# Performance work log

Measured on AMD Instinct MI355X. Metric: run time of the kernel, lower is better.

The kernel has to match this reference:

```python
import math
import jax, jax.numpy as jnp
import numpy as np

B, L, D, H, NL, V = 4, 1024, 1024, 16, 8, 32000
HD = D // H
EPS = 1e-5


def _sinusoidal_pe(length, dim):
    pos = jnp.arange(length, dtype=jnp.float32)[:, None]
    div = jnp.exp(jnp.arange(0, dim, 2, dtype=jnp.float32) * (-math.log(10000.0) / dim))
    pe = jnp.zeros((length, dim), dtype=jnp.float32)
    pe = pe.at[:, 0::2].set(jnp.sin(pos * div))
    pe = pe.at[:, 1::2].set(jnp.cos(pos * div))
    return pe


def _layer_norm(x, scale, bias):
    mu = jnp.mean(x, axis=-1, keepdims=True)
    var = jnp.mean(jnp.square(x - mu), axis=-1, keepdims=True)
    return (x - mu) * jax.lax.rsqrt(var + EPS) * scale + bias


def setup_inputs() -> dict:
    key = jax.random.key(0)
    ks = jax.random.split(key, 10)
    std = 0.02
    p = {
        "idx": jax.random.randint(ks[0], (B, L), 0, V),
        "emb": jax.random.normal(ks[1], (V, D), jnp.float32) * std,
        # per-layer stacked params (leading dim NL)
        "ln1_s": jnp.ones((NL, D), jnp.float32),
        "ln1_b": jnp.zeros((NL, D), jnp.float32),
        "wq": jax.random.normal(ks[2], (NL, D, D), jnp.float32) * std,
        "wk": jax.random.normal(ks[3], (NL, D, D), jnp.float32) * std,
        "wv": jax.random.normal(ks[4], (NL, D, D), jnp.float32) * std,
        "wo": jax.random.normal(ks[5], (NL, D, D), jnp.float32) * std,
        "ln2_s": jnp.ones((NL, D), jnp.float32),
        "ln2_b": jnp.zeros((NL, D), jnp.float32),
        "w1": jax.random.normal(ks[6], (NL, D, 4 * D), jnp.float32) * std,
        "b1": jnp.zeros((NL, 4 * D), jnp.float32),
        "w2": jax.random.normal(ks[7], (NL, 4 * D, D), jnp.float32) * std,
        "b2": jnp.zeros((NL, D), jnp.float32),
        "lnf_s": jnp.ones((D,), jnp.float32),
        "lnf_b": jnp.zeros((D,), jnp.float32),
        "head": jax.random.normal(ks[8], (D, V), jnp.float32) * std,
    }
    return p


def _forward(idx, emb, ln1_s, ln1_b, wq, wk, wv, wo, ln2_s, ln2_b, w1, b1, w2, b2, lnf_s, lnf_b, head):
    x = emb[idx] + _sinusoidal_pe(L, D)[None]  # [B,L,D]
    causal = jnp.tril(jnp.ones((L, L), dtype=bool))  # [L,L]
    neg_inf = jnp.float32(-jnp.inf)

    def block(x, p):
        (l1s, l1b, Wq, Wk, Wv, Wo, l2s, l2b, W1, B1, W2, B2) = p
        h = _layer_norm(x, l1s, l1b)
        q = (h @ Wq).reshape(B, L, H, HD)
        k = (h @ Wk).reshape(B, L, H, HD)
        v = (h @ Wv).reshape(B, L, H, HD)
        att = jnp.einsum("bihd,bjhd->bhij", q, k) / math.sqrt(HD)
        att = jnp.where(causal, att, neg_inf)
        att = jax.nn.softmax(att, axis=-1)
        y = jnp.einsum("bhij,bjhd->bihd", att, v).reshape(B, L, D)
        x = x + y @ Wo
        h = _layer_norm(x, l2s, l2b)
        x = x + jax.nn.gelu(h @ W1 + B1, approximate=False) @ W2 + B2
        return x, None

    params = (ln1_s, ln1_b, wq, wk, wv, wo, ln2_s, ln2_b, w1, b1, w2, b2)
    x, _ = jax.lax.scan(block, x, params)
    x = _layer_norm(x, lnf_s, lnf_b)
    return x @ head  # [B,L,V]


def reference(idx, emb, ln1_s, ln1_b, wq, wk, wv, wo, ln2_s, ln2_b, w1, b1, w2, b2, lnf_s, lnf_b, head):
    return _forward(idx, emb, ln1_s, ln1_b, wq, wk, wv, wo, ln2_s, ln2_b, w1, b1, w2, b2, lnf_s, lnf_b, head)
```

## Files before the change

kernel.cpp:

```cpp
#include <hip/hip_runtime.h>
#include <hip/hip_bf16.h>
#include <math.h>

typedef __bf16 bf16_t;
typedef __attribute__((ext_vector_type(8))) __bf16 bf16x8;
typedef __attribute__((ext_vector_type(4))) float f32x4;

#define B_  4
#define L_  1024
#define D_  1024
#define H_  16
#define HD_ 64
#define NL_ 8
#define V_  32000
#define FF_ 4096

__global__ __launch_bounds__(256) void embed_kernel(const int* __restrict__ idx,
                                                    const float* __restrict__ emb,
                                                    float* __restrict__ x) {
  int token = blockIdx.x;
  int l = token & (L_ - 1);
  int id = idx[token];
  const float* erow = emb + (size_t)id * D_;
  float* xrow = x + (size_t)token * D_;
  int d0 = threadIdx.x * 4;
#pragma unroll
  for (int j = 0; j < 4; ++j) {
    int d = d0 + j;
    int i = d >> 1;
    float freq = expf((float)(2 * i) * (-9.210340371976184f / (float)D_));
    float ang = (float)l * freq;
    float pe = (d & 1) ? cosf(ang) : sinf(ang);
    xrow[d] = erow[d] + pe;
  }
}

__global__ __launch_bounds__(256) void ln_kernel(const float* __restrict__ x,
                                                 const float* __restrict__ gamma,
                                                 const float* __restrict__ beta,
                                                 bf16_t* __restrict__ out) {
  int row = blockIdx.x;
  int t = threadIdx.x;
  float4 v = ((const float4*)(x + (size_t)row * D_))[t];
  float va[4] = {v.x, v.y, v.z, v.w};
  float s = va[0] + va[1] + va[2] + va[3];
  float ss = va[0]*va[0] + va[1]*va[1] + va[2]*va[2] + va[3]*va[3];
#pragma unroll
  for (int m = 1; m < 64; m <<= 1) {
    s  += __shfl_xor(s, m);
    ss += __shfl_xor(ss, m);
  }
  __shared__ float red[8];
  int wid = t >> 6, lane = t & 63;
  if (lane == 0) { red[wid] = s; red[4 + wid] = ss; }
  __syncthreads();
  s  = red[0] + red[1] + red[2] + red[3];
  ss = red[4] + red[5] + red[6] + red[7];
  float mu  = s * (1.0f / D_);
  float var = fmaxf(ss * (1.0f / D_) - mu * mu, 0.0f);
  float rstd = rsqrtf(var + 1e-5f);
  int d0 = t * 4;
  bf16_t* orow = out + (size_t)row * D_ + d0;
#pragma unroll
  for (int j = 0; j < 4; ++j) {
    int d = d0 + j;
    orow[j] = (bf16_t)((va[j] - mu) * rstd * gamma[d] + beta[d]);
  }
}

__global__ void transpose_k(const float* __restrict__ in, size_t base,
                            bf16_t* __restrict__ out, int K, int N, int ldin) {
  __shared__ bf16_t tile[32][33];
  int n0 = blockIdx.x * 32, k0 = blockIdx.y * 32;
#pragma unroll
  for (int r = 0; r < 4; ++r) {
    int kk = threadIdx.y + r * 8;
    tile[kk][threadIdx.x] = (bf16_t)in[base + (size_t)(k0 + kk) * ldin + n0 + threadIdx.x];
  }
  __syncthreads();
#pragma unroll
  for (int r = 0; r < 4; ++r) {
    int nn = threadIdx.y + r * 8;
    out[(size_t)(n0 + nn) * K + k0 + threadIdx.x] = tile[threadIdx.x][nn];
  }
}

__global__ void transpose_qkv(const float* __restrict__ wq,
                              const float* __restrict__ wk,
                              const float* __restrict__ wv, size_t base,
                              bf16_t* __restrict__ out) {
  const float* in = (blockIdx.z == 0) ? wq : (blockIdx.z == 1) ? wk : wv;
  __shared__ bf16_t tile[32][33];
  int n0 = blockIdx.x * 32, k0 = blockIdx.y * 32;
#pragma unroll
  for (int r = 0; r < 4; ++r) {
    int kk = threadIdx.y + r * 8;
    tile[kk][threadIdx.x] = (bf16_t)in[base + (size_t)(k0 + kk) * D_ + n0 + threadIdx.x];
  }
  __syncthreads();
  bf16_t* o = out + (size_t)blockIdx.z * D_ * D_;
#pragma unroll
  for (int r = 0; r < 4; ++r) {
    int nn = threadIdx.y + r * 8;
    o[(size_t)(n0 + nn) * D_ + k0 + threadIdx.x] = tile[threadIdx.x][nn];
  }
}

__device__ __forceinline__ void gload_lds16(const bf16_t* g, bf16_t* lds) {
  __builtin_amdgcn_global_load_lds(
      (const __attribute__((address_space(1))) void*)g,
      (__attribute__((address_space(3))) void*)(void*)lds,
      16, 0, 0);
}

__device__ __forceinline__ void remap_block(int& bn, int& bm) {
  const int gx = gridDim.x, gy = gridDim.y;
  int lin = blockIdx.y * gx + blockIdx.x;
  int nwg = gx * gy;
  int q8 = nwg >> 3, r8 = nwg & 7;
  int xcd = lin & 7, pos = lin >> 3;
  int wg = (xcd < r8 ? xcd * (q8 + 1) : r8 * (q8 + 1) + (xcd - r8) * q8) + pos;
  if ((gy & 7) == 0) {
    int per = gx << 3;
    int grp = wg / per, win = wg % per;
    bm = (grp << 3) + (win & 7);
    bn = win >> 3;
  } else { bn = wg % gx; bm = wg / gx; }
}

template <int EPI>
__global__ __launch_bounds__(256) void gemm_bt_kernel(
    const bf16_t* __restrict__ A, const bf16_t* __restrict__ Bt,
    bf16_t* __restrict__ outb, float* __restrict__ outf,
    const float* __restrict__ bias, int M, int Nst, int K, int col0) {
  int bn, bm; remap_block(bn, bm);
  const int tid = threadIdx.x, wid = tid >> 6, lane = tid & 63;
  const int wm = wid >> 1, wn = wid & 1;
  const int l15 = lane & 15, l4 = lane >> 4;

  __shared__ __align__(16) bf16_t As[128 * 32];
  __shared__ __align__(16) bf16_t Bs[128 * 32];

  f32x4 acc[4][4] = {};

  const bf16_t* Ablk = A  + (size_t)(bm * 128) * K;
  const bf16_t* Bblk = Bt + (size_t)(bn * 128) * K;
  const int srow = lane >> 2;
  const int skof = (lane & 3) * 8;

  for (int k0 = 0; k0 < K; k0 += 32) {
#pragma unroll
    for (int c = 0; c < 2; ++c) {
      int chunk = wid * 2 + c;
      int row = chunk * 16 + srow;
      gload_lds16(Ablk + (size_t)row * K + k0 + skof, As + chunk * 512);
      gload_lds16(Bblk + (size_t)row * K + k0 + skof, Bs + chunk * 512);
    }
    __syncthreads();

    bf16x8 af[4], bfv[4];
#pragma unroll
    for (int i = 0; i < 4; ++i)
      af[i] = *(const bf16x8*)(As + (wm * 64 + i * 16 + l15) * 32 + l4 * 8);
#pragma unroll
    for (int j = 0; j < 4; ++j)
      bfv[j] = *(const bf16x8*)(Bs + (wn * 64 + j * 16 + l15) * 32 + l4 * 8);
#pragma unroll
    for (int i = 0; i < 4; ++i)
#pragma unroll
      for (int j = 0; j < 4; ++j)
        acc[i][j] = __builtin_amdgcn_mfma_f32_16x16x32_bf16(af[i], bfv[j], acc[i][j], 0, 0, 0);
    __syncthreads();
  }

  const int row_base = bm * 128 + wm * 64;
  const int col_base = col0 + bn * 128 + wn * 64 + l15;
#pragma unroll
  for (int i = 0; i < 4; ++i) {
#pragma unroll
    for (int j = 0; j < 4; ++j) {
      int col = col_base + j * 16;
#pragma unroll
      for (int r = 0; r < 4; ++r) {
        int row = row_base + i * 16 + l4 * 4 + r;
        float val = acc[i][j][r];
        if (EPI == 1) {
          outf[(size_t)row * Nst + col] += val;
        } else {
          outf[(size_t)row * Nst + col] += val + bias[col];
        }
      }
    }
  }
}

template <int EPI>
__global__ __launch_bounds__(512, 2) void gemm256_kernel(
    const bf16_t* __restrict__ A, const bf16_t* __restrict__ Bt,
    bf16_t* __restrict__ outb, float* __restrict__ outf,
    const float* __restrict__ bias, int M, int Nst, int K, int col0) {
  int bn, bm; remap_block(bn, bm);
  const int tid = threadIdx.x, wid = tid >> 6, lane = tid & 63;
  const int wm = wid >> 2, wn = wid & 3;
  const int l15 = lane & 15, l4 = lane >> 4;

  __shared__ __align__(16) bf16_t smem[65536];

  f32x4 acc[8][4] = {};

  const bf16_t* Ab = A  + (size_t)(bm * 256) * K;
  const bf16_t* Bb = Bt + (size_t)(bn * 256) * K;
  const int NT = K >> 6;

  const int srow = tid >> 3;
  const int sx8  = tid & 7;
  const int xrd  = l15 & 7;

  auto stage_rows = [&](int t, int mat, int R) {
    const bf16_t* g = mat ? Bb : Ab;
    bf16_t* l = smem + (t & 1) * 32768 + mat * 16384 + R * 64;
    int row = R + srow;
    int gs  = sx8 ^ (row & 7);
    gload_lds16(g + (size_t)row * K + t * 64 + gs * 8, l + wid * 512);
  };
  auto stA_SP0 = [&](int t) { stage_rows(t, 0, 0);   stage_rows(t, 0, 128); };
  auto stA_SP1 = [&](int t) { stage_rows(t, 0, 64);  stage_rows(t, 0, 192); };
  auto stB_H0  = [&](int t) { stage_rows(t, 1, 0);   stage_rows(t, 1, 64);  };
  auto stB_H1  = [&](int t) { stage_rows(t, 1, 128); stage_rows(t, 1, 192); };

  stA_SP0(0); stB_H0(0); stA_SP1(0); stB_H1(0);
  stA_SP0(1); stB_H0(1); stA_SP1(1);
  asm volatile("s_waitcnt vmcnt(6)" ::: "memory");
  __builtin_amdgcn_s_barrier();

  bf16x8 af[4][2], bfr[4][2];

  auto rdB = [&](const bf16_t* sB, int nh) {
#pragma unroll
    for (int n = 0; n < 2; ++n)
#pragma unroll
      for (int ks = 0; ks < 2; ++ks)
        bfr[nh * 2 + n][ks] = *(const bf16x8*)(sB + (wn * 64 + (nh * 2 + n) * 16 + l15) * 64
                                                  + ((ks * 4 + l4) ^ xrd) * 8);
  };
  auto rdA = [&](const bf16_t* sA, int mh) {
#pragma unroll
    for (int m = 0; m < 4; ++m)
#pragma unroll
      for (int ks = 0; ks < 2; ++ks)
        af[m][ks] = *(const bf16x8*)(sA + (wm * 128 + mh * 64 + m * 16 + l15) * 64
                                        + ((ks * 4 + l4) ^ xrd) * 8);
  };
  auto mma = [&](int mh, int nh) {
    asm volatile("s_waitcnt lgkmcnt(0)" ::: "memory");
    __builtin_amdgcn_sched_barrier(0);
    __builtin_amdgcn_s_setprio(1);
#pragma unroll
    for (int m = 0; m < 4; ++m)
#pragma unroll
      for (int n = 0; n < 2; ++n)
#pragma unroll
        for (int ks = 0; ks < 2; ++ks)
          acc[mh * 4 + m][nh * 2 + n] = __builtin_amdgcn_mfma_f32_16x16x32_bf16(
              af[m][ks], bfr[nh * 2 + n][ks], acc[mh * 4 + m][nh * 2 + n], 0, 0, 0);
    __builtin_amdgcn_s_setprio(0);
  };

  const int NI = NT >> 1;
  for (int it = 0; it < NI; ++it) {
    const int T0 = 2 * it, T1 = 2 * it + 1;
    const bool pre = (it + 1 < NI);
    const bf16_t* sA0 = smem;
    const bf16_t* sB0 = smem + 16384;
    const bf16_t* sA1 = smem + 32768;
    const bf16_t* sB1 = smem + 49152;

    rdB(sB0, 0); rdA(sA0, 0);
    stB_H1(T1);
    __builtin_amdgcn_s_barrier();
    mma(0, 0);
    __builtin_amdgcn_s_barrier();
    rdB(sB0, 1);
    if (pre) stA_SP0(T0 + 2);
    __builtin_amdgcn_s_barrier();
    mma(0, 1);
    __builtin_amdgcn_s_barrier();
    rdA(sA0, 1);
    if (pre) stB_H0(T0 + 2);
    __builtin_amdgcn_s_barrier();
    mma(1, 0);
    __builtin_amdgcn_s_barrier();
    if (pre) stA_SP1(T0 + 2);
    __builtin_amdgcn_s_barrier();
    mma(1, 1);
    if (pre) { asm volatile("s_waitcnt vmcnt(6)" ::: "memory"); }
    else     { asm volatile("s_waitcnt vmcnt(0)" ::: "memory"); }
    __builtin_amdgcn_s_barrier();

    rdB(sB1, 0); rdA(sA1, 0);
    if (pre) stB_H1(T0 + 2);
    __builtin_amdgcn_s_barrier();
    mma(0, 0);
    __builtin_amdgcn_s_barrier();
    rdB(sB1, 1);
    if (pre) stA_SP0(T1 + 2);
    __builtin_amdgcn_s_barrier();
    mma(0, 1);
    __builtin_amdgcn_s_barrier();
    rdA(sA1, 1);
    if (pre) stB_H0(T1 + 2);
    __builtin_amdgcn_s_barrier();
    mma(1, 0);
    __builtin_amdgcn_s_barrier();
    if (pre) stA_SP1(T1 + 2);
    __builtin_amdgcn_s_barrier();
    mma(1, 1);
    if (pre) { asm volatile("s_waitcnt vmcnt(6)" ::: "memory"); }
    __builtin_amdgcn_s_barrier();
  }

  const int row_base = bm * 256 + wm * 128;
#pragma unroll
  for (int m = 0; m < 8; ++m) {
#pragma unroll
    for (int n = 0; n < 4; ++n) {
      int colg = bn * 256 + wn * 64 + n * 16 + l15;
#pragma unroll
      for (int r = 0; r < 4; ++r) {
        int row = row_base + m * 16 + l4 * 4 + r;
        float val = acc[m][n][r];
        if (EPI == 4) {
          outf[(size_t)row * Nst + col0 + colg] = val;
        } else if (EPI == 2) {
          int col = col0 + colg;
          float v2 = val + bias[col];
          v2 = 0.5f * v2 * (1.0f + erff(v2 * 0.7071067811865475f));
          outb[(size_t)row * Nst + col] = (bf16_t)v2;
        } else {
          int buf = colg >> 10;
          int lc  = colg & 1023;
          (outb + (size_t)buf * 4194304)[(size_t)row * 1024 + lc] = (bf16_t)val;
        }
      }
    }
  }
}

__global__ __launch_bounds__(256) void attn_kernel(
    const bf16_t* __restrict__ q, const bf16_t* __restrict__ k,
    const bf16_t* __restrict__ v, bf16_t* __restrict__ y) {
  int bid = blockIdx.x;
  int qt = bid & 15;
  int h  = (bid >> 4) & (H_ - 1);
  int b  = bid >> 8;
  int tid = threadIdx.x, wid = tid >> 6, lane = tid & 63;
  int l15 = lane & 15, l4 = lane >> 4;

  __shared__ __align__(16) bf16_t Ks[64 * 72];
  __shared__ __align__(16) bf16_t Vs[64 * 72];
  __shared__ __align__(16) bf16_t Ps[4][16 * 72];

  const int qrow0 = qt * 64 + wid * 16;
  const size_t bh = ((size_t)b * L_ * H_ + h) * HD_;

  bf16x8 qf[2];
#pragma unroll
  for (int c = 0; c < 2; ++c)
    qf[c] = *(const bf16x8*)(q + bh + (size_t)(qrow0 + l15) * (H_ * HD_) + c * 32 + l4 * 8);

  float m_r[4] = {-INFINITY, -INFINITY, -INFINITY, -INFINITY};
  float l_r[4] = {0.f, 0.f, 0.f, 0.f};
  f32x4 oacc[4] = {};

  for (int kt = 0; kt <= qt; ++kt) {
    __syncthreads();
    int kbase = kt * 64;
#pragma unroll
    for (int s = 0; s < 2; ++s) {
      int seg = s * 256 + tid;
      int j = seg >> 3;
      int dof = (seg & 7) * 8;
      const size_t src = bh + (size_t)(kbase + j) * (H_ * HD_) + dof;
      *(bf16x8*)(Ks + j * 72 + dof) = *(const bf16x8*)(k + src);
      bf16x8 vv = *(const bf16x8*)(v + src);
      int colb = (j + dof) & 63;
#pragma unroll
      for (int jj = 0; jj < 8; ++jj) Vs[(dof + jj) * 72 + colb] = vv[jj];
    }
    __syncthreads();

    f32x4 sacc[4] = {};
#pragma unroll
    for (int c = 0; c < 2; ++c) {
#pragma unroll
      for (int t = 0; t < 4; ++t) {
        bf16x8 kf = *(const bf16x8*)(Ks + (t * 16 + l15) * 72 + c * 32 + l4 * 8);
        sacc[t] = __builtin_amdgcn_mfma_f32_16x16x32_bf16(qf[c], kf, sacc[t], 0, 0, 0);
      }
    }

    float tmax[4] = {-INFINITY, -INFINITY, -INFINITY, -INFINITY};
#pragma unroll
    for (int t = 0; t < 4; ++t) {
#pragma unroll
      for (int r = 0; r < 4; ++r) {
        float sv = sacc[t][r] * 0.125f;
        int kj = kbase + t * 16 + l15;
        int qi = qrow0 + l4 * 4 + r;
        if (kj > qi) sv = -INFINITY;
        sacc[t][r] = sv;
        tmax[r] = fmaxf(tmax[r], sv);
      }
    }
#pragma unroll
    for (int r = 0; r < 4; ++r) {
#pragma unroll
      for (int md = 1; md < 16; md <<= 1)
        tmax[r] = fmaxf(tmax[r], __shfl_xor(tmax[r], md));
    }
    float alpha[4], tsum[4];
#pragma unroll
    for (int r = 0; r < 4; ++r) {
      float mn = fmaxf(m_r[r], tmax[r]);
      alpha[r] = expf(m_r[r] - mn);
      m_r[r] = mn;
      tsum[r] = 0.f;
    }
#pragma unroll
    for (int t = 0; t < 4; ++t) {
#pragma unroll
      for (int r = 0; r < 4; ++r) {
        float p = expf(sacc[t][r] - m_r[r]);
        tsum[r] += p;
        Ps[wid][(l4 * 4 + r) * 72 + t * 16 + l15] = (bf16_t)p;
      }
    }
#pragma unroll
    for (int r = 0; r < 4; ++r) {
#pragma unroll
      for (int md = 1; md < 16; md <<= 1)
        tsum[r] += __shfl_xor(tsum[r], md);
      l_r[r] = l_r[r] * alpha[r] + tsum[r];
    }
#pragma unroll
    for (int t = 0; t < 4; ++t)
#pragma unroll
      for (int r = 0; r < 4; ++r)
        oacc[t][r] *= alpha[r];

#pragma unroll
    for (int c = 0; c < 2; ++c) {
      bf16x8 pf = *(const bf16x8*)(&Ps[wid][l15 * 72 + c * 32 + l4 * 8]);
#pragma unroll
      for (int t = 0; t < 4; ++t) {
        int d = t * 16 + l15;
        int jb = c * 32 + l4 * 8;
        bf16x8 vf = *(const bf16x8*)(Vs + d * 72 + ((jb + (d & 56)) & 63));
        oacc[t] = __builtin_amdgcn_mfma_f32_16x16x32_bf16(pf, vf, oacc[t], 0, 0, 0);
      }
    }
  }

#pragma unroll
  for (int t = 0; t < 4; ++t) {
#pragma unroll
    for (int r = 0; r < 4; ++r) {
      int row = qrow0 + l4 * 4 + r;
      int d = t * 16 + l15;
      y[bh + (size_t)row * (H_ * HD_) + d] = (bf16_t)(oacc[t][r] / l_r[r]);
    }
  }
}

extern "C" void kernel_launch(void* const* d_in, const int* in_sizes, int n_in,
                              void* d_out, int out_size, void* d_ws, size_t ws_size,
                              hipStream_t stream) {
  (void)in_sizes; (void)n_in; (void)out_size;
  const int*   idx   = (const int*)d_in[0];
  const float* emb   = (const float*)d_in[1];
  const float* ln1_s = (const float*)d_in[2];
  const float* ln1_b = (const float*)d_in[3];
  const float* wq    = (const float*)d_in[4];
  const float* wk    = (const float*)d_in[5];
  const float* wv    = (const float*)d_in[6];
  const float* wo    = (const float*)d_in[7];
  const float* ln2_s = (const float*)d_in[8];
  const float* ln2_b = (const float*)d_in[9];
  const float* w1    = (const float*)d_in[10];
  const float* b1    = (const float*)d_in[11];
  const float* w2    = (const float*)d_in[12];
  const float* b2    = (const float*)d_in[13];
  const float* lnf_s = (const float*)d_in[14];
  const float* lnf_b = (const float*)d_in[15];
  const float* headw = (const float*)d_in[16];
  float* out = (float*)d_out;

  char* ws = (char*)d_ws;
  const size_t XO  = 0;
  const size_t HBO = XO  + 16777216;
  const size_t QBO = HBO + 8388608;
  const size_t KBO = QBO + 8388608;
  const size_t VBO = KBO + 8388608;
  const size_t YBO = VBO + 8388608;
  const size_t GBO = QBO;
  const size_t WTO = YBO + 8388608;

  float*  X  = (float*)(ws + XO);
  bf16_t* Hb = (bf16_t*)(ws + HBO);
  bf16_t* Qb = (bf16_t*)(ws + QBO);
  bf16_t* Kb = (bf16_t*)(ws + KBO);
  bf16_t* Vb = (bf16_t*)(ws + VBO);
  bf16_t* Yb = (bf16_t*)(ws + YBO);
  bf16_t* Gb = (bf16_t*)(ws + GBO);
  bf16_t* WT = (bf16_t*)(ws + WTO);

  const int M = B_ * L_;
  const dim3 tb(32, 8);

  embed_kernel<<<M, 256, 0, stream>>>(idx, emb, X);

  for (int l = 0; l < NL_; ++l) {
    const size_t wof = (size_t)l * D_ * D_;
    ln_kernel<<<M, 256, 0, stream>>>(X, ln1_s + (size_t)l * D_, ln1_b + (size_t)l * D_, Hb);

    transpose_qkv<<<dim3(D_/32, D_/32, 3), tb, 0, stream>>>(wq, wk, wv, wof, WT);
    gemm256_kernel<5><<<dim3(3*D_/256, M/256), 512, 0, stream>>>(Hb, WT, Qb, nullptr, nullptr, M, D_, D_, 0);

    attn_kernel<<<B_ * H_ * (L_/64), 256, 0, stream>>>(Qb, Kb, Vb, Yb);

    transpose_k<<<dim3(D_/32, D_/32), tb, 0, stream>>>(wo, wof, WT, D_, D_, D_);
    gemm_bt_kernel<1><<<dim3(D_/128, M/128), 256, 0, stream>>>(Yb, WT, nullptr, X, nullptr, M, D_, D_, 0);

    ln_kernel<<<M, 256, 0, stream>>>(X, ln2_s + (size_t)l * D_, ln2_b + (size_t)l * D_, Hb);

    transpose_k<<<dim3(FF_/32, D_/32), tb, 0, stream>>>(w1, (size_t)l * D_ * FF_, WT, D_, FF_, FF_);
    gemm256_kernel<2><<<dim3(FF_/256, M/256), 512, 0, stream>>>(Hb, WT, Gb, nullptr, b1 + (size_t)l * FF_, M, FF_, D_, 0);

    transpose_k<<<dim3(D_/32, FF_/32), tb, 0, stream>>>(w2, (size_t)l * FF_ * D_, WT, FF_, D_, D_);
    gemm_bt_kernel<3><<<dim3(D_/128, M/128), 256, 0, stream>>>(Gb, WT, nullptr, X, b2 + (size_t)l * D_, M, D_, FF_, 0);
  }

  ln_kernel<<<M, 256, 0, stream>>>(X, lnf_s, lnf_b, Hb);

  size_t avail = (ws_size > WTO) ? (ws_size - WTO) : 0;
  long long maxcols = (long long)(avail / ((size_t)D_ * 2));
  int chunk = (int)((maxcols / 256) * 256);
  if (chunk > V_) chunk = V_;
  if (chunk < 256) chunk = 256;
  for (int n0 = 0; n0 < V_; n0 += chunk) {
    int nc = (V_ - n0 < chunk) ? (V_ - n0) : chunk;
    transpose_k<<<dim3(nc/32, D_/32), tb, 0, stream>>>(headw, (size_t)n0, WT, D_, nc, V_);
    gemm256_kernel<4><<<dim3(nc/256, M/256), 512, 0, stream>>>(Hb, WT, nullptr, out, nullptr, M, V_, D_, n0);
  }
}
```

Before: 3.037 ms.

## Fuse per-layer weight transposes and split-K the narrow GEMMs with atomics

All per-layer weight transposes (QKV, Wo, W1, W2) now run in a single kernel launch into separate workspace buffers, replacing four launches per layer. The two 1024-column residual GEMMs (Wo and W2) gain a split-K grid dimension of 2 and 4 and accumulate into the residual with float atomicAdd, with the bias added only by the first split. This gives the 256-block grids more blocks to fill the GPU. The cost is atomic traffic and non-deterministic summation order.

```diff
diff --git a/kernel.cpp b/kernel.cpp
--- a/kernel.cpp
+++ b/kernel.cpp
@@ -85,24 +85,44 @@
   }
 }
 
-__global__ void transpose_qkv(const float* __restrict__ wq,
-                              const float* __restrict__ wk,
-                              const float* __restrict__ wv, size_t base,
-                              bf16_t* __restrict__ out) {
-  const float* in = (blockIdx.z == 0) ? wq : (blockIdx.z == 1) ? wk : wv;
+__global__ void transpose_layer(const float* __restrict__ wq, const float* __restrict__ wk,
+                                const float* __restrict__ wv, const float* __restrict__ wo,
+                                const float* __restrict__ w1, const float* __restrict__ w2,
+                                size_t wofD, size_t wofF,
+                                bf16_t* __restrict__ qkvT, bf16_t* __restrict__ woT,
+                                bf16_t* __restrict__ w1T, bf16_t* __restrict__ w2T) {
+  int t = blockIdx.x;
+  const float* in; bf16_t* out; int K, N, ldin, x, y;
+  if (t < 3072) {
+    int z = t >> 10, tt = t & 1023;
+    in = (z == 0 ? wq : z == 1 ? wk : wv) + wofD;
+    out = qkvT + (size_t)z * D_ * D_;
+    K = D_; N = D_; ldin = D_; x = tt & 31; y = tt >> 5;
+  } else if (t < 4096) {
+    int tt = t - 3072;
+    in = wo + wofD; out = woT;
+    K = D_; N = D_; ldin = D_; x = tt & 31; y = tt >> 5;
+  } else if (t < 8192) {
+    int tt = t - 4096;
+    in = w1 + wofF; out = w1T;
+    K = D_; N = FF_; ldin = FF_; x = tt & 127; y = tt >> 7;
+  } else {
+    int tt = t - 8192;
+    in = w2 + wofF; out = w2T;
+    K = FF_; N = D_; ldin = D_; x = tt & 31; y = tt >> 5;
+  }
   __shared__ bf16_t tile[32][33];
-  int n0 = blockIdx.x * 32, k0 = blockIdx.y * 32;
+  int n0 = x * 32, k0 = y * 32;
 #pragma unroll
   for (int r = 0; r < 4; ++r) {
     int kk = threadIdx.y + r * 8;
-    tile[kk][threadIdx.x] = (bf16_t)in[base + (size_t)(k0 + kk) * D_ + n0 + threadIdx.x];
+    tile[kk][threadIdx.x] = (bf16_t)in[(size_t)(k0 + kk) * ldin + n0 + threadIdx.x];
   }
   __syncthreads();
-  bf16_t* o = out + (size_t)blockIdx.z * D_ * D_;
 #pragma unroll
   for (int r = 0; r < 4; ++r) {
     int nn = threadIdx.y + r * 8;
-    o[(size_t)(n0 + nn) * D_ + k0 + threadIdx.x] = tile[threadIdx.x][nn];
+    out[(size_t)(n0 + nn) * K + k0 + threadIdx.x] = tile[threadIdx.x][nn];
   }
 }
 
@@ -134,6 +154,9 @@
     bf16_t* __restrict__ outb, float* __restrict__ outf,
     const float* __restrict__ bias, int M, int Nst, int K, int col0) {
   int bn, bm; remap_block(bn, bm);
+  const int kz = blockIdx.z, KS = gridDim.z;
+  const int Kc = K / KS;
+  const int kbeg = kz * Kc, kend = kbeg + Kc;
   const int tid = threadIdx.x, wid = tid >> 6, lane = tid & 63;
   const int wm = wid >> 1, wn = wid & 1;
   const int l15 = lane & 15, l4 = lane >> 4;
@@ -148,7 +171,7 @@
   const int srow = lane >> 2;
   const int skof = (lane & 3) * 8;
 
-  for (int k0 = 0; k0 < K; k0 += 32) {
+  for (int k0 = kbeg; k0 < kend; k0 += 32) {
 #pragma unroll
     for (int c = 0; c < 2; ++c) {
       int chunk = wid * 2 + c;
@@ -184,11 +207,8 @@
       for (int r = 0; r < 4; ++r) {
         int row = row_base + i * 16 + l4 * 4 + r;
         float val = acc[i][j][r];
-        if (EPI == 1) {
-          outf[(size_t)row * Nst + col] += val;
-        } else {
-          outf[(size_t)row * Nst + col] += val + bias[col];
-        }
+        if (EPI == 3 && kz == 0) val += bias[col];
+        atomicAdd(&outf[(size_t)row * Nst + col], val);
       }
     }
   }
@@ -504,15 +524,24 @@
   const size_t YBO = VBO + 8388608;
   const size_t GBO = QBO;
   const size_t WTO = YBO + 8388608;
-
-  float*  X  = (float*)(ws + XO);
-  bf16_t* Hb = (bf16_t*)(ws + HBO);
-  bf16_t* Qb = (bf16_t*)(ws + QBO);
-  bf16_t* Kb = (bf16_t*)(ws + KBO);
-  bf16_t* Vb = (bf16_t*)(ws + VBO);
-  bf16_t* Yb = (bf16_t*)(ws + YBO);
-  bf16_t* Gb = (bf16_t*)(ws + GBO);
-  bf16_t* WT = (bf16_t*)(ws + WTO);
+  const size_t QKVT = WTO;
+  const size_t WOT  = QKVT + 6291456;
+  const size_t W1T  = WOT + 2097152;
+  const size_t W2T  = W1T + 8388608;
+  const size_t HDT  = WTO;
+
+  float*  X   = (float*)(ws + XO);
+  bf16_t* Hb  = (bf16_t*)(ws + HBO);
+  bf16_t* Qb  = (bf16_t*)(ws + QBO);
+  bf16_t* Kb  = (bf16_t*)(ws + KBO);
+  bf16_t* Vb  = (bf16_t*)(ws + VBO);
+  bf16_t* Yb  = (bf16_t*)(ws + YBO);
+  bf16_t* Gb  = (bf16_t*)(ws + GBO);
+  bf16_t* qkvT = (bf16_t*)(ws + QKVT);
+  bf16_t* woT  = (bf16_t*)(ws + WOT);
+  bf16_t* w1T  = (bf16_t*)(ws + W1T);
+  bf16_t* w2T  = (bf16_t*)(ws + W2T);
+  bf16_t* WT   = (bf16_t*)(ws + HDT);
 
   const int M = B_ * L_;
   const dim3 tb(32, 8);
@@ -520,29 +549,30 @@
   embed_kernel<<<M, 256, 0, stream>>>(idx, emb, X);
 
   for (int l = 0; l < NL_; ++l) {
-    const size_t wof = (size_t)l * D_ * D_;
+    const size_t wofD = (size_t)l * D_ * D_;
+    const size_t wofF = (size_t)l * D_ * FF_;
+
     ln_kernel<<<M, 256, 0, stream>>>(X, ln1_s + (size_t)l * D_, ln1_b + (size_t)l * D_, Hb);
 
-    transpose_qkv<<<dim3(D_/32, D_/32, 3), tb, 0, stream>>>(wq, wk, wv, wof, WT);
-    gemm256_kernel<5><<<dim3(3*D_/256, M/256), 512, 0, stream>>>(Hb, WT, Qb, nullptr, nullptr, M, D_, D_, 0);
+    transpose_layer<<<12288, tb, 0, stream>>>(wq, wk, wv, wo, w1, w2, wofD, wofF,
+                                              qkvT, woT, w1T, w2T);
+
+    gemm256_kernel<5><<<dim3(3*D_/256, M/256), 512, 0, stream>>>(Hb, qkvT, Qb, nullptr, nullptr, M, D_, D_, 0);
 
     attn_kernel<<<B_ * H_ * (L_/64), 256, 0, stream>>>(Qb, Kb, Vb, Yb);
 
-    transpose_k<<<dim3(D_/32, D_/32), tb, 0, stream>>>(wo, wof, WT, D_, D_, D_);
-    gemm_bt_kernel<1><<<dim3(D_/128, M/128), 256, 0, stream>>>(Yb, WT, nullptr, X, nullptr, M, D_, D_, 0);
+    gemm_bt_kernel<1><<<dim3(D_/128, M/128, 2), 256, 0, stream>>>(Yb, woT, nullptr, X, nullptr, M, D_, D_, 0);
 
     ln_kernel<<<M, 256, 0, stream>>>(X, ln2_s + (size_t)l * D_, ln2_b + (size_t)l * D_, Hb);
 
-    transpose_k<<<dim3(FF_/32, D_/32), tb, 0, stream>>>(w1, (size_t)l * D_ * FF_, WT, D_, FF_, FF_);
-    gemm256_kernel<2><<<dim3(FF_/256, M/256), 512, 0, stream>>>(Hb, WT, Gb, nullptr, b1 + (size_t)l * FF_, M, FF_, D_, 0);
-
-    transpose_k<<<dim3(D_/32, FF_/32), tb, 0, stream>>>(w2, (size_t)l * FF_ * D_, WT, FF_, D_, D_);
-    gemm_bt_kernel<3><<<dim3(D_/128, M/128), 256, 0, stream>>>(Gb, WT, nullptr, X, b2 + (size_t)l * D_, M, D_, FF_, 0);
+    gemm256_kernel<2><<<dim3(FF_/256, M/256), 512, 0, stream>>>(Hb, w1T, Gb, nullptr, b1 + (size_t)l * FF_, M, FF_, D_, 0);
+
+    gemm_bt_kernel<3><<<dim3(D_/128, M/128, 4), 256, 0, stream>>>(Gb, w2T, nullptr, X, b2 + (size_t)l * D_, M, D_, FF_, 0);
   }
 
   ln_kernel<<<M, 256, 0, stream>>>(X, lnf_s, lnf_b, Hb);
 
-  size_t avail = (ws_size > WTO) ? (ws_size - WTO) : 0;
+  size_t avail = (ws_size > HDT) ? (ws_size - HDT) : 0;
   long long maxcols = (long long)(avail / ((size_t)D_ * 2));
   int chunk = (int)((maxcols / 256) * 256);
   if (chunk > V_) chunk = V_;
```

Result: faster. 2.934 ms (-3.4%).
